# Kernel optimization log

Measured on AMD Instinct MI355X. Metric: run time of the kernel, lower is better.

## Reference

```python
import jax, jax.numpy as jnp
import numpy as np
import math

HEADS = 4
DK = 64            # dim // heads
TEMP = 1.0
LMAX = 2048        # max segment length (for padded ragged attention)


def setup_inputs() -> dict:
    key = jax.random.key(0)
    ks = jax.random.split(key, 6)
    T, H, B = 1024, 256, 16
    # ragged lengths alternating 2048/1024 -> N = 24576
    lengths = np.tile(np.array([2048, 1024], dtype=np.int64), B // 2)
    N = int(lengths.sum())
    s = 1.0 / math.sqrt(H)
    return {
        "go_mat": jax.random.normal(ks[0], (T, H), jnp.float32),
        "node_h": jax.random.normal(ks[1], (N, H), jnp.float32),
        "Wq": jax.random.normal(ks[2], (H, H), jnp.float32) * s,
        "Wk": jax.random.normal(ks[3], (H, H), jnp.float32) * s,
        "Wv": jax.random.normal(ks[4], (H, H), jnp.float32) * s,
        "Wproj": jax.random.normal(ks[5], (H, H), jnp.float32) * s,
        "num_nodes_per_graph": jnp.asarray(lengths),
    }


def reference(go_mat, node_h, Wq, Wk, Wv, Wproj, num_nodes_per_graph):
    lengths = num_nodes_per_graph
    B = lengths.shape[0]
    N, H = node_h.shape
    T = go_mat.shape[0]

    # segment bookkeeping: graph id and within-graph offset for each node
    cum = jnp.cumsum(lengths)                       # [B]
    starts = cum - lengths                          # [B]
    g = jnp.searchsorted(cum, jnp.arange(N), side="right")  # [N] graph id
    off = jnp.arange(N) - starts[g]                 # [N] position within graph

    # projections (torch Linear: x @ W.T)
    Q = (go_mat @ Wq.T).reshape(T, HEADS, DK).transpose(1, 0, 2)   # [h,T,dk]
    K = node_h @ Wk.T                                              # [N,H]
    V = node_h @ Wv.T

    # scatter packed nodes into padded [B, Lmax, H]
    Kp = jnp.zeros((B, LMAX, H), K.dtype).at[g, off].set(K)
    Vp = jnp.zeros((B, LMAX, H), V.dtype).at[g, off].set(V)
    Kp = Kp.reshape(B, LMAX, HEADS, DK).transpose(0, 2, 1, 3)      # [B,h,L,dk]
    Vp = Vp.reshape(B, LMAX, HEADS, DK).transpose(0, 2, 1, 3)

    scores = jnp.einsum("htd,bhld->bhtl", Q, Kp) / (math.sqrt(DK) * TEMP)
    valid = jnp.arange(LMAX)[None, :] < lengths[:, None]           # [B,L]
    scores = jnp.where(valid[:, None, None, :], scores, jnp.float32(-1e30))
    attn = jax.nn.softmax(scores, axis=-1)                         # [B,h,T,L]

    ctx = jnp.einsum("bhtl,bhld->bhtd", attn, Vp)                  # [B,h,T,dk]
    ctx = ctx.transpose(0, 2, 1, 3).reshape(B, T, H)               # [B,T,H]
    return ctx @ Wproj.T
```

## Files before the change

kernel.cpp:

```cpp
#include <hip/hip_runtime.h>
#include <math.h>

#define HEADS 4
#define DK 64
#define HD 256

typedef __attribute__((ext_vector_type(8))) __bf16 bf16x8;
typedef __attribute__((ext_vector_type(4))) float floatx4;

__device__ __forceinline__ ushort f2bf(float f) {
  union { float f; unsigned u; } x; x.f = f;
  return (ushort)((x.u + 0x7FFF + ((x.u >> 16) & 1)) >> 16);
}

#if __has_builtin(__builtin_amdgcn_exp2f)
#define EXP2(x) __builtin_amdgcn_exp2f(x)
#else
#define EXP2(x) exp2f(x)
#endif

__device__ __forceinline__ unsigned cvtpk_bf16(float lo, float hi) {
  unsigned r;
  asm("v_cvt_pk_bf16_f32 %0, %1, %2" : "=v"(r) : "v"(lo), "v"(hi));
  return r;
}

#define GLDS(g, l) __builtin_amdgcn_global_load_lds(                      \
    (const __attribute__((address_space(1))) unsigned*)(g),               \
    (__attribute__((address_space(3))) unsigned*)(l), 16, 0, 0)

__global__ __launch_bounds__(256) void cvt_fused(
    const float* __restrict__ go, const float* __restrict__ nh,
    const float* __restrict__ w0, const float* __restrict__ w1,
    const float* __restrict__ w2, const float* __restrict__ w3,
    ushort* __restrict__ gobf, ushort* __restrict__ nodebf,
    ushort* __restrict__ wbf, int T, int N) {
  const int idx = blockIdx.x * 256 + threadIdx.x;
  const int row = idx >> 5, gr = idx & 31;
  if (row >= T + N + 4 * 256) return;
  const float* x; ushort* y; int r = row;
  if (row < T) { x = go; y = gobf; }
  else if (row < T + N) { x = nh; y = nodebf; r = row - T; }
  else {
    const int wr = row - T - N, wi = wr >> 8;
    r = wr & 255;
    x = (wi == 0) ? w0 : (wi == 1) ? w1 : (wi == 2) ? w2 : w3;
    y = wbf + (size_t)wi * HD * HD;
  }
  const int chunk = gr >> 3, g = gr & 7;
  const float* src = x + (size_t)r * 256 + gr * 8;
  float4 a = *(const float4*)src;
  float4 bq = *(const float4*)(src + 4);
  ushort* dst = y + (size_t)r * 256 + chunk * 64 + (g ^ (r & 7)) * 8;
  union { ushort4 h[2]; uint4 q; } pk;
  pk.h[0] = (ushort4){f2bf(a.x), f2bf(a.y), f2bf(a.z), f2bf(a.w)};
  pk.h[1] = (ushort4){f2bf(bq.x), f2bf(bq.y), f2bf(bq.z), f2bf(bq.w)};
  *(uint4*)dst = pk.q;
}

template <int NW>
__device__ __forceinline__ void gemm_tile(const ushort* __restrict__ A,
                                          const ushort* __restrict__ W,
                                          ushort* __restrict__ C, int m0,
                                          int n0, int mode, int ldc,
                                          ushort* As, ushort* Ws, int lane,
                                          int w, int quad, int l15) {
  const int wm = w & 1, wn = w >> 1;
  floatx4 acc[4][NW];
#pragma unroll
  for (int mt = 0; mt < 4; ++mt)
#pragma unroll
    for (int nt = 0; nt < NW; ++nt) acc[mt][nt] = (floatx4){0.f, 0.f, 0.f, 0.f};

  for (int k0 = 0; k0 < 256; k0 += 64) {
    __syncthreads();
#pragma unroll
    for (int t = 0; t < 4; ++t)
      GLDS(A + (size_t)(m0 + w * 32 + t * 8 + (lane >> 3)) * 256 + k0 + (lane & 7) * 8,
           &As[(w * 32 + t * 8) * 64]);
#pragma unroll
    for (int t = 0; t < NW; ++t)
      GLDS(W + (size_t)(n0 + w * (8 * NW) + t * 8 + (lane >> 3)) * 256 + k0 + (lane & 7) * 8,
           &Ws[(w * (8 * NW) + t * 8) * 64]);
    __syncthreads();

#pragma unroll
    for (int kk = 0; kk < 2; ++kk) {
      const int pg = ((kk * 4 + quad) ^ (l15 & 7)) * 8;
      bf16x8 af[4], bfr[NW];
#pragma unroll
      for (int mt = 0; mt < 4; ++mt)
        af[mt] = *(const bf16x8*)&As[(wm * 64 + mt * 16 + l15) * 64 + pg];
#pragma unroll
      for (int nt = 0; nt < NW; ++nt)
        bfr[nt] = *(const bf16x8*)&Ws[(wn * (16 * NW) + nt * 16 + l15) * 64 + pg];
#pragma unroll
      for (int mt = 0; mt < 4; ++mt)
#pragma unroll
        for (int nt = 0; nt < NW; ++nt)
          acc[mt][nt] = __builtin_amdgcn_mfma_f32_16x16x32_bf16(
              af[mt], bfr[nt], acc[mt][nt], 0, 0, 0);
    }
  }

#pragma unroll
  for (int mt = 0; mt < 4; ++mt)
#pragma unroll
    for (int nt = 0; nt < NW; ++nt) {
      const int col = n0 + wn * (16 * NW) + nt * 16 + l15;
      if (mode == 2) {
        const int d = col & 63;
        const int g = mt * 2 + (quad >> 1);
        const int node = m0 + wm * 64 + (g ^ (d & 7)) * 8 + (quad & 1) * 4;
        ushort4 o = {f2bf(acc[mt][nt][0]), f2bf(acc[mt][nt][1]),
                     f2bf(acc[mt][nt][2]), f2bf(acc[mt][nt][3])};
        *(ushort4*)&C[(size_t)col * ldc + node] = o;
      } else {
#pragma unroll
        for (int r = 0; r < 4; ++r) {
          const int row = m0 + wm * 64 + mt * 16 + quad * 4 + r;
          int cc = col;
          if (mode == 1)
            cc = (col & ~63) | (((((col >> 3) & 7) ^ (row & 7))) << 3) | (col & 7);
          C[(size_t)row * 256 + cc] = f2bf(acc[mt][nt][r]);
        }
      }
    }
}

__global__ __launch_bounds__(256) void qkv_gemm(const ushort* __restrict__ gobf,
                                                const ushort* __restrict__ nodebf,
                                                const ushort* __restrict__ wbf,
                                                ushort* __restrict__ Qbf,
                                                ushort* __restrict__ Kgb,
                                                ushort* __restrict__ Vtb,
                                                int T, int N) {
  __shared__ __align__(16) ushort As[128 * 64];
  __shared__ __align__(16) ushort Ws[128 * 64];
  const int tid = threadIdx.x, lane = tid & 63, w = tid >> 6;
  const int quad = lane >> 4, l15 = lane & 15;
  const int QX = T >> 7, KB = N >> 7;
  const int NT = QX + 2 * KB;
  const int jx = blockIdx.x % NT;
  const int n0 = (blockIdx.x / NT) * 128;
  if (jx < QX)
    gemm_tile<4>(gobf, wbf, Qbf, jx * 128, n0, 0, 0, As, Ws, lane, w, quad, l15);
  else if (jx < QX + KB)
    gemm_tile<4>(nodebf, wbf + (size_t)HD * HD, Kgb, (jx - QX) * 128, n0, 1, 0,
                 As, Ws, lane, w, quad, l15);
  else
    gemm_tile<4>(nodebf, wbf + (size_t)2 * HD * HD, Vtb, (jx - QX - KB) * 128,
                 n0, 2, N, As, Ws, lane, w, quad, l15);
}

__global__ __launch_bounds__(256, 3) void attn_split(
    const ushort* __restrict__ Qb, const ushort* __restrict__ Kg,
    const ushort* __restrict__ Vt, const int* __restrict__ lens,
    float* __restrict__ Opart, float* __restrict__ Lpart,
    int T, int N, int B) {
  __shared__ __align__(16) ushort Ks[2][64 * 64];
  __shared__ __align__(16) ushort Vs[2][64 * 64];

  const int tid = threadIdx.x, lane = tid & 63, wave = tid >> 6;
  const int quad = lane >> 4, l15 = lane & 15;
  const int QX = T >> 7;
  const int nspl = N >> 10;
  const int grpc = HEADS * nspl;
  const int qx = blockIdx.x / grpc;
  const int rem = blockIdx.x - qx * grpc;
  const int h = rem / nspl;
  const int zid = rem - h * nspl;

  int z = zid, b, start = 0, len = 0, off = -1;
  for (b = 0; b < B; ++b) {
    len = lens[b];
    const int s = (len + 1023) >> 10;
    if (z < s) { off = z << 10; break; }
    z -= s; start += len;
  }
  if (off < 0) return;
  const int kcnt = min(1024, len - off);
  const int kbeg = start + off;

  for (int i = (int)(blockIdx.x >> 8); i > 0; --i)
    __builtin_amdgcn_s_sleep(35);

  const int q0 = qx * 128 + wave * 32;
  bf16x8 qb[2][2];
#pragma unroll
  for (int qt = 0; qt < 2; ++qt)
#pragma unroll
    for (int kk = 0; kk < 2; ++kk)
      qb[qt][kk] = *(const bf16x8*)(Qb + (size_t)(q0 + qt * 16 + l15) * 256 +
                                    h * 64 + kk * 32 + quad * 8);

  floatx4 o[2][4];
#pragma unroll
  for (int qt = 0; qt < 2; ++qt)
#pragma unroll
    for (int nt = 0; nt < 4; ++nt) o[qt][nt] = (floatx4){0.f, 0.f, 0.f, 0.f};
  float lsum[2] = {0.f, 0.f};

  const float sc = 0.18033688011112042f;
  const int srow = lane >> 3;
  const int scol = (lane & 7) * 8;

  GLDS(Kg + (size_t)(kbeg + wave * 8 + srow) * 256 + h * 64 + scol,
       &Ks[0][(wave * 8) * 64]);
  GLDS(Kg + (size_t)(kbeg + wave * 8 + 32 + srow) * 256 + h * 64 + scol,
       &Ks[0][(wave * 8 + 32) * 64]);
  GLDS(Vt + (size_t)(h * 64 + wave * 8 + srow) * (size_t)N + kbeg + scol,
       &Vs[0][(wave * 8) * 64]);
  GLDS(Vt + (size_t)(h * 64 + wave * 8 + 32 + srow) * (size_t)N + kbeg + scol,
       &Vs[0][(wave * 8 + 32) * 64]);

  int buf = 0;
  for (int j0 = 0; j0 < kcnt; j0 += 64, buf ^= 1) {
    __syncthreads();
    const int jn = j0 + 64;
    if (jn < kcnt) {
      GLDS(Kg + (size_t)(kbeg + jn + wave * 8 + srow) * 256 + h * 64 + scol,
           &Ks[buf ^ 1][(wave * 8) * 64]);
      GLDS(Kg + (size_t)(kbeg + jn + wave * 8 + 32 + srow) * 256 + h * 64 + scol,
           &Ks[buf ^ 1][(wave * 8 + 32) * 64]);
      GLDS(Vt + (size_t)(h * 64 + wave * 8 + srow) * (size_t)N + kbeg + jn + scol,
           &Vs[buf ^ 1][(wave * 8) * 64]);
      GLDS(Vt + (size_t)(h * 64 + wave * 8 + 32 + srow) * (size_t)N + kbeg + jn + scol,
           &Vs[buf ^ 1][(wave * 8 + 32) * 64]);
    }

    floatx4 st[4][2];
#pragma unroll
    for (int t = 0; t < 4; ++t)
#pragma unroll
      for (int qt = 0; qt < 2; ++qt) st[t][qt] = (floatx4){0.f, 0.f, 0.f, 0.f};
    __builtin_amdgcn_s_setprio(1);
#pragma unroll
    for (int kk = 0; kk < 2; ++kk) {
#pragma unroll
      for (int t = 0; t < 4; ++t) {
        bf16x8 kf = *(const bf16x8*)&Ks[buf][(t * 16 + l15) * 64 +
                                            ((kk * 4 + quad) ^ (l15 & 7)) * 8];
        st[t][0] = __builtin_amdgcn_mfma_f32_16x16x32_bf16(kf, qb[0][kk], st[t][0], 0, 0, 0);
        st[t][1] = __builtin_amdgcn_mfma_f32_16x16x32_bf16(kf, qb[1][kk], st[t][1], 0, 0, 0);
      }
    }
    __builtin_amdgcn_s_setprio(0);

    unsigned W[4][2][2];
    if (jn <= kcnt) {
#pragma unroll
      for (int t = 0; t < 4; ++t)
#pragma unroll
        for (int qt = 0; qt < 2; ++qt) {
          float p[4];
#pragma unroll
          for (int r = 0; r < 4; ++r) p[r] = EXP2(fmaf(st[t][qt][r], sc, -32.0f));
          lsum[qt] += (p[0] + p[1]) + (p[2] + p[3]);
          W[t][qt][0] = cvtpk_bf16(p[0], p[1]);
          W[t][qt][1] = cvtpk_bf16(p[2], p[3]);
        }
    } else {
#pragma unroll
      for (int t = 0; t < 4; ++t)
#pragma unroll
        for (int qt = 0; qt < 2; ++qt) {
          float p[4];
#pragma unroll
          for (int r = 0; r < 4; ++r) {
            const bool v = (j0 + t * 16 + quad * 4 + r) < kcnt;
            p[r] = v ? EXP2(fmaf(st[t][qt][r], sc, -32.0f)) : 0.0f;
          }
          lsum[qt] += (p[0] + p[1]) + (p[2] + p[3]);
          W[t][qt][0] = cvtpk_bf16(p[0], p[1]);
          W[t][qt][1] = cvtpk_bf16(p[2], p[3]);
        }
    }

#pragma unroll
    for (int ks = 0; ks < 2; ++ks) {
      bf16x8 pa[2];
#pragma unroll
      for (int qt = 0; qt < 2; ++qt) {
        unsigned a0 = W[2 * ks][qt][0], a1 = W[2 * ks][qt][1];
        unsigned b0 = W[2 * ks + 1][qt][0], b1 = W[2 * ks + 1][qt][1];
        asm("v_permlane32_swap_b32 %0, %1" : "+v"(a0), "+v"(b0));
        asm("v_permlane32_swap_b32 %0, %1" : "+v"(a1), "+v"(b1));
        asm("v_permlane16_swap_b32 %0, %1" : "+v"(a0), "+v"(b0));
        asm("v_permlane16_swap_b32 %0, %1" : "+v"(a1), "+v"(b1));
        union { uint4 u; bf16x8 v; } c;
        c.u = make_uint4(a0, a1, b0, b1);
        pa[qt] = c.v;
      }
      __builtin_amdgcn_s_setprio(1);
#pragma unroll
      for (int nt = 0; nt < 4; ++nt) {
        bf16x8 vf = *(const bf16x8*)&Vs[buf][(nt * 16 + l15) * 64 +
                                            ((ks * 4 + quad) ^ (l15 & 7)) * 8];
        o[0][nt] = __builtin_amdgcn_mfma_f32_16x16x32_bf16(pa[0], vf, o[0][nt], 0, 0, 0);
        o[1][nt] = __builtin_amdgcn_mfma_f32_16x16x32_bf16(pa[1], vf, o[1][nt], 0, 0, 0);
      }
      __builtin_amdgcn_s_setprio(0);
    }
  }

  const int part = (zid * HEADS + h) * QX + qx;
  float* op = Opart + (size_t)part * 8192;
#pragma unroll
  for (int qt = 0; qt < 2; ++qt) {
#pragma unroll
    for (int nt = 0; nt < 4; ++nt)
#pragma unroll
      for (int r = 0; r < 4; ++r)
        op[(wave * 32 + qt * 16 + quad * 4 + r) * 64 + nt * 16 + l15] = o[qt][nt][r];
    float lt = lsum[qt];
    lt += __shfl_xor(lt, 16);
    lt += __shfl_xor(lt, 32);
    if (lane < 16)
      Lpart[(size_t)part * 128 + wave * 32 + qt * 16 + lane] = lt;
  }
}

__global__ __launch_bounds__(256) void combine_proj(
    const float* __restrict__ Opart, const float* __restrict__ Lpart,
    const int* __restrict__ lens, const ushort* __restrict__ wproj,
    float* __restrict__ outp, int T) {
  __shared__ __align__(16) ushort Cs[32 * 256];
  __shared__ __align__(16) ushort Ws[64 * 256];

  const int t = threadIdx.x;
  {
    const int lrow = t >> 3;
    const int h = (t >> 1) & 3;
    const int half = t & 1;
    const int row = blockIdx.x * 32 + lrow;
    const int b = row / T;
    const int tq = row - b * T;
    const int qx = tq >> 7, qr = tq & 127;
    const int QX = T >> 7;
    int z0 = 0;
    for (int i = 0; i < b; ++i) z0 += (lens[i] + 1023) >> 10;
    const int ns = (lens[b] + 1023) >> 10;

    float l = 0.f;
    float4 acc[8];
#pragma unroll
    for (int g = 0; g < 8; ++g) acc[g] = make_float4(0.f, 0.f, 0.f, 0.f);
    for (int s = 0; s < ns; ++s) {
      const size_t part = (size_t)((z0 + s) * HEADS + h) * QX + qx;
      l += Lpart[part * 128 + qr];
      const float4* src = (const float4*)(Opart + part * 8192 + (size_t)qr * 64) +
                          half * 8;
#pragma unroll
      for (int g = 0; g < 8; ++g) {
        float4 v = src[g];
        acc[g].x += v.x; acc[g].y += v.y; acc[g].z += v.z; acc[g].w += v.w;
      }
    }
    const float inv = 1.0f / l;
    ushort* dst = &Cs[lrow * 256 + h * 64];
#pragma unroll
    for (int g2 = 0; g2 < 4; ++g2) {
      const int gg = half * 4 + g2;
      const float4 a = acc[g2 * 2], c = acc[g2 * 2 + 1];
      const int phys = gg ^ (lrow & 7);
      ushort4 o0 = {f2bf(a.x * inv), f2bf(a.y * inv), f2bf(a.z * inv), f2bf(a.w * inv)};
      ushort4 o1 = {f2bf(c.x * inv), f2bf(c.y * inv), f2bf(c.z * inv), f2bf(c.w * inv)};
      *(ushort4*)&dst[phys * 8] = o0;
      *(ushort4*)&dst[phys * 8 + 4] = o1;
    }
  }

  const int lane = t & 63, w = t >> 6;
  const int quad = lane >> 4, l15 = lane & 15;
  const int rt = (w & 1) * 16;
  const int ct = (w >> 1) * 32;
  const size_t row0 = (size_t)blockIdx.x * 32;

  for (int n0c = 0; n0c < 256; n0c += 64) {
    __syncthreads();
#pragma unroll
    for (int tt = 0; tt < 8; ++tt)
      GLDS(wproj + (size_t)(n0c + w * 16 + tt * 2 + (lane >> 5)) * 256 + (lane & 31) * 8,
           &Ws[(w * 16 + tt * 2) * 256]);
    __syncthreads();

    floatx4 oacc[2];
#pragma unroll
    for (int nt = 0; nt < 2; ++nt) oacc[nt] = (floatx4){0.f, 0.f, 0.f, 0.f};
#pragma unroll
    for (int c = 0; c < 4; ++c)
#pragma unroll
      for (int kk = 0; kk < 2; ++kk) {
        const int pg = ((kk * 4 + quad) ^ (l15 & 7)) * 8;
        bf16x8 af = *(const bf16x8*)&Cs[(rt + l15) * 256 + c * 64 + pg];
#pragma unroll
        for (int nt = 0; nt < 2; ++nt) {
          bf16x8 bfr = *(const bf16x8*)&Ws[(ct + nt * 16 + l15) * 256 + c * 64 + pg];
          oacc[nt] = __builtin_amdgcn_mfma_f32_16x16x32_bf16(af, bfr, oacc[nt], 0, 0, 0);
        }
      }
#pragma unroll
    for (int nt = 0; nt < 2; ++nt)
#pragma unroll
      for (int r = 0; r < 4; ++r)
        outp[(row0 + rt + quad * 4 + r) * 256 + n0c + ct + nt * 16 + l15] = oacc[nt][r];
  }
}

extern "C" void kernel_launch(void* const* d_in, const int* in_sizes, int n_in,
                              void* d_out, int out_size, void* d_ws, size_t ws_size,
                              hipStream_t stream) {
  const float* go     = (const float*)d_in[0];
  const float* node_h = (const float*)d_in[1];
  const float* Wq     = (const float*)d_in[2];
  const float* Wk     = (const float*)d_in[3];
  const float* Wv     = (const float*)d_in[4];
  const float* Wproj  = (const float*)d_in[5];
  const int*   lens   = (const int*)d_in[6];

  const int T = in_sizes[0] / HD;
  const int N = in_sizes[1] / HD;
  const int B = in_sizes[6];
  const int NSPL = N >> 10;
  const int QX = T >> 7;
  const int KB = N >> 7;

  char* p = (char*)d_ws;
  ushort* Kgb  = (ushort*)p;  p += (size_t)N * HD * 2;
  ushort* Vtb  = (ushort*)p;  p += (size_t)N * HD * 2;
  ushort* Qbf  = (ushort*)p;  p += (size_t)T * HD * 2;
  ushort* gobf = (ushort*)p;  p += (size_t)T * HD * 2;
  ushort* ctxb = (ushort*)p;  p += (size_t)B * T * HD * 2;
  ushort* wbf  = (ushort*)p;  p += (size_t)4 * HD * HD * 2;
  ushort* nodebf = (ushort*)p;
  float* Opart = (float*)p;   p += (size_t)NSPL * HEADS * QX * 8192 * 4;
  float* Lpart = (float*)p;   p += (size_t)NSPL * HEADS * QX * 128 * 4;
  (void)ctxb;

  cvt_fused<<<((T + N + 1024) * 32 + 255) / 256, 256, 0, stream>>>(
      go, node_h, Wq, Wk, Wv, Wproj, gobf, nodebf, wbf, T, N);

  qkv_gemm<<<(QX + 2 * KB) * 2, 256, 0, stream>>>(gobf, nodebf, wbf, Qbf, Kgb,
                                                  Vtb, T, N);

  attn_split<<<QX * HEADS * NSPL, 256, 0, stream>>>(Qbf, Kgb, Vtb, lens,
                                                    Opart, Lpart, T, N, B);

  combine_proj<<<(B * T) / 32, 256, 0, stream>>>(Opart, Lpart, lens,
                                                 wbf + (size_t)3 * HD * HD,
                                                 (float*)d_out, T);
}
```

Measured before the change: 151.8 us.

## Double-buffer Wproj tiles and remap combine blocks across XCDs

```diff
diff --git a/kernel.cpp b/kernel.cpp
--- a/kernel.cpp
+++ b/kernel.cpp
@@ -324,18 +324,47 @@
 __global__ __launch_bounds__(256) void combine_proj(
     const float* __restrict__ Opart, const float* __restrict__ Lpart,
     const int* __restrict__ lens, const ushort* __restrict__ wproj,
-    float* __restrict__ outp, int T) {
+    float* __restrict__ outp, int T, int B) {
   __shared__ __align__(16) ushort Cs[32 * 256];
-  __shared__ __align__(16) ushort Ws[64 * 256];
+  __shared__ __align__(16) ushort Ws[2][64 * 256];
 
   const int t = threadIdx.x;
+  const int lane = t & 63, w = t >> 6;
+  const int bps = T >> 5;
+
+  int b = -1, local = 0;
+  if (B == 16 && bps == 32 && gridDim.x == 512) {
+    int z = 0; unsigned cnt2 = 0, cnt1 = 0; bool ok = true;
+    for (int bb = 0; bb < 16; ++bb) {
+      const int rr = z & 7;
+      if (cnt1 & (1u << rr)) { if (cnt2 & (1u << rr)) ok = false; else cnt2 |= 1u << rr; }
+      else cnt1 |= 1u << rr;
+      z += (lens[bb] + 1023) >> 10;
+    }
+    if (ok && cnt2 == 0xFFu) {
+      const int r = (int)(blockIdx.x & 7), j = (int)(blockIdx.x >> 3);
+      const int which = j >> 5;
+      local = j & 31;
+      int cnt = 0; z = 0;
+      for (int bb = 0; bb < 16; ++bb) {
+        if ((z & 7) == r) { if (cnt == which) b = bb; ++cnt; }
+        z += (lens[bb] + 1023) >> 10;
+      }
+    }
+  }
+  if (b < 0) { b = blockIdx.x / bps; local = blockIdx.x % bps; }
+  const int row_base = b * T + local * 32;
+
+#pragma unroll
+  for (int tt = 0; tt < 8; ++tt)
+    GLDS(wproj + (size_t)(w * 16 + tt * 2 + (lane >> 5)) * 256 + (lane & 31) * 8,
+         &Ws[0][(w * 16 + tt * 2) * 256]);
+
   {
     const int lrow = t >> 3;
     const int h = (t >> 1) & 3;
     const int half = t & 1;
-    const int row = blockIdx.x * 32 + lrow;
-    const int b = row / T;
-    const int tq = row - b * T;
+    const int tq = local * 32 + lrow;
     const int qx = tq >> 7, qr = tq & 127;
     const int QX = T >> 7;
     int z0 = 0;
@@ -371,19 +400,21 @@
     }
   }
 
-  const int lane = t & 63, w = t >> 6;
   const int quad = lane >> 4, l15 = lane & 15;
   const int rt = (w & 1) * 16;
   const int ct = (w >> 1) * 32;
-  const size_t row0 = (size_t)blockIdx.x * 32;
-
-  for (int n0c = 0; n0c < 256; n0c += 64) {
+  const size_t row0 = (size_t)row_base;
+
+  int buf = 0;
+  for (int n0c = 0; n0c < 256; n0c += 64, buf ^= 1) {
     __syncthreads();
-#pragma unroll
-    for (int tt = 0; tt < 8; ++tt)
-      GLDS(wproj + (size_t)(n0c + w * 16 + tt * 2 + (lane >> 5)) * 256 + (lane & 31) * 8,
-           &Ws[(w * 16 + tt * 2) * 256]);
-    __syncthreads();
+    const int nn = n0c + 64;
+    if (nn < 256) {
+#pragma unroll
+      for (int tt = 0; tt < 8; ++tt)
+        GLDS(wproj + (size_t)(nn + w * 16 + tt * 2 + (lane >> 5)) * 256 + (lane & 31) * 8,
+             &Ws[buf ^ 1][(w * 16 + tt * 2) * 256]);
+    }
 
     floatx4 oacc[2];
 #pragma unroll
@@ -396,7 +427,7 @@
         bf16x8 af = *(const bf16x8*)&Cs[(rt + l15) * 256 + c * 64 + pg];
 #pragma unroll
         for (int nt = 0; nt < 2; ++nt) {
-          bf16x8 bfr = *(const bf16x8*)&Ws[(ct + nt * 16 + l15) * 256 + c * 64 + pg];
+          bf16x8 bfr = *(const bf16x8*)&Ws[buf][(ct + nt * 16 + l15) * 256 + c * 64 + pg];
           oacc[nt] = __builtin_amdgcn_mfma_f32_16x16x32_bf16(af, bfr, oacc[nt], 0, 0, 0);
         }
       }
@@ -449,5 +480,5 @@
 
   combine_proj<<<(B * T) / 32, 256, 0, stream>>>(Opart, Lpart, lens,
                                                  wbf + (size_t)3 * HD * HD,
-                                                 (float*)d_out, T);
-}
+                                                 (float*)d_out, T, B);
+}
```

After: 154.1 us. Within noise of the previous version (+1.5%).
